# Kernel tuning notes

Measured on AMD Instinct MI355X. Metric: run time of the kernel, lower is better.

## Reference

```python
import jax, jax.numpy as jnp
import numpy as np

B, N, C = 32, 4097, 256  # N odd so threshold length (N+1)//2 == N//2+1 rfft bins
F = N // 2 + 1


def setup_inputs() -> dict:
    key = jax.random.key(0)
    k1, k2, k3, k4 = jax.random.split(key, 4)
    x_in = jax.random.normal(k1, (B, N, C), dtype=jnp.float32)
    # trunc_normal(std=0.02) ~ scaled normal for reference purposes
    complex_weight = jax.random.normal(k2, (C, 2), dtype=jnp.float32) * 0.02
    complex_weight_high = jax.random.normal(k3, (C, 2), dtype=jnp.float32) * 0.02
    threshold_param = jax.random.uniform(k4, (F,), dtype=jnp.float32)
    return {
        "x_in": x_in,
        "complex_weight": complex_weight,
        "complex_weight_high": complex_weight_high,
        "threshold_param": threshold_param,
    }


def reference(x_in, complex_weight, complex_weight_high, threshold_param):
    dtype = x_in.dtype
    x = x_in.astype(jnp.float32)
    x_fft = jnp.fft.rfft(x, axis=1, norm="ortho")  # [B, F, C] complex64

    weight = complex_weight[:, 0] + 1j * complex_weight[:, 1]  # [C]
    x_weighted = x_fft * weight

    # adaptive high-frequency mask (straight-through on threshold_param)
    energy = jnp.sum(jnp.abs(x_fft) ** 2, axis=-1)  # [B, F]
    median_energy = jnp.median(energy, axis=1, keepdims=True)  # [B, 1] (F odd -> exact middle, matches torch)
    normalized_energy = energy / (median_energy + 1e-6)
    hard = (normalized_energy > threshold_param).astype(jnp.float32)  # [B, F]
    adaptive_mask = jax.lax.stop_gradient(hard - threshold_param) + threshold_param

    weight_high = complex_weight_high[:, 0] + 1j * complex_weight_high[:, 1]  # [C]
    x_weighted = x_weighted + x_fft * adaptive_mask[..., None] * weight_high

    out = jnp.fft.irfft(x_weighted, n=N, axis=1, norm="ortho")  # [B, N, C]
    return out.astype(dtype)
```

## Files before the change

### kernel.cpp

```cpp
#include <hip/hip_runtime.h>
#include <math.h>
#include <float.h>

#define B_ 32
#define N_ 4097
#define C_ 256
#define F_ 2049
#define N2_ 241
#define Q_ 512
#define TWROWS 4352
#define INV_SQRT_N 0.0156230927f
#define W_N 0.0015336063f
#define W_17 0.36959913571644626f

typedef __attribute__((ext_vector_type(8))) short short8v;
typedef _Float16 f16x8 __attribute__((ext_vector_type(8)));
typedef __attribute__((ext_vector_type(4))) float f32x4;

#define C17T(r) ((r)==0 ? 1.0f : (r)==1 ? 0.9324722294f : (r)==2 ? 0.7390089172f : \
    (r)==3 ? 0.4457383558f : (r)==4 ? 0.0922683595f : (r)==5 ? -0.2736629901f : \
    (r)==6 ? -0.6026346364f : (r)==7 ? -0.8502171357f : (r)==8 ? -0.9829730997f : \
    (r)==9 ? -0.9829730997f : (r)==10 ? -0.8502171357f : (r)==11 ? -0.6026346364f : \
    (r)==12 ? -0.2736629901f : (r)==13 ? 0.0922683595f : (r)==14 ? 0.4457383558f : \
    (r)==15 ? 0.7390089172f : 0.9324722294f)
#define S17T(r) ((r)==0 ? 0.0f : (r)==1 ? 0.3612416662f : (r)==2 ? 0.6736956436f : \
    (r)==3 ? 0.8951632914f : (r)==4 ? 0.9957341763f : (r)==5 ? 0.9618256432f : \
    (r)==6 ? 0.7980172273f : (r)==7 ? 0.5264321629f : (r)==8 ? 0.1837495178f : \
    (r)==9 ? -0.1837495178f : (r)==10 ? -0.5264321629f : (r)==11 ? -0.7980172273f : \
    (r)==12 ? -0.9618256432f : (r)==13 ? -0.9957341763f : (r)==14 ? -0.8951632914f : \
    (r)==15 ? -0.6736956436f : -0.3612416662f)

__device__ __forceinline__ float bf2f(unsigned short u) {
    return __uint_as_float(((unsigned)u) << 16);
}
__device__ __forceinline__ unsigned short f2bf(float v) {
    unsigned u = __float_as_uint(v);
    u += 0x7FFFu + ((u >> 16) & 1u);
    return (unsigned short)(u >> 16);
}
__device__ __forceinline__ unsigned short f2h(float v) {
    union { _Float16 h; unsigned short u; } cv;
    cv.h = (_Float16)v;
    return cv.u;
}
__device__ __forceinline__ void gload16(const void* gptr, void* ldsptr) {
    __builtin_amdgcn_global_load_lds(
        (const __attribute__((address_space(1))) void*)gptr,
        (__attribute__((address_space(3))) void*)ldsptr,
        16, 0, 0);
}

__global__ __launch_bounds__(256, 4) void k_prep(const float* __restrict__ x,
                                                 unsigned short* __restrict__ yt,
                                                 unsigned short* __restrict__ twA,
                                                 unsigned short* __restrict__ twB) {
    int blk = blockIdx.x;
    int tid = threadIdx.x;
    if (blk >= 2048) {
        int base = (blk - 2048) * 4;
#pragma unroll
        for (int u = 0; u < 4; ++u) {
            int g = base + u;
            if (g < TWROWS) {
                int n = g, k2 = tid;
                unsigned pack = 0u;
                if (n <= 4096 && k2 <= 240) {
                    int rr = (n * k2) % N_;
                    float s, cth; sincosf(W_N * (float)rr, &s, &cth);
                    pack = (unsigned)f2bf(cth) | ((unsigned)f2bf(-s) << 16);
                }
                *(unsigned*)(twA + (size_t)n * Q_ + 2 * k2) = pack;
            } else {
                int i2 = g - TWROWS;
                int m = i2 & 255; int k1 = i2 >> 8;
                int n2 = tid;
                int t = m >> 1, r = m & 1;
                int f = k1 + 17 * t;
                unsigned ph = 0u;
                if (t <= 120 && f < F_ && n2 <= 240) {
                    float s_ = (k1 <= 8) ? 1.f : -1.f;
                    int rr = (f * n2) % N_;
                    float sn, cs; sincosf(W_N * (float)rr, &sn, &cs);
                    float a0 = (r == 0) ? cs : -sn;
                    float a1 = (r == 0) ? s_ * sn : s_ * cs;
                    ph = (unsigned)f2h(a0) | ((unsigned)f2h(a1) << 16);
                }
                size_t ub = ((size_t)(k1 * 256 + m)) * 256 + n2;
                *((unsigned*)twB + ub) = ph;
            }
        }
        return;
    }

    int b = blk >> 6; int rem = blk & 63;
    int n2t = rem >> 2, ct = rem & 3;
    int cl = tid & 63, sub = tid >> 6;
    int c = ct * 64 + cl;

    float ar[9][4], ai[8][4];
#pragma unroll
    for (int k = 0; k < 9; ++k)
#pragma unroll
        for (int i = 0; i < 4; ++i) ar[k][i] = 0.f;
#pragma unroll
    for (int k = 0; k < 8; ++k)
#pragma unroll
        for (int i = 0; i < 4; ++i) ai[k][i] = 0.f;

    const float* xb = x + (size_t)b * N_ * C_ + c;
#pragma unroll
    for (int n1 = 0; n1 < 17; ++n1) {
        float xv[4];
#pragma unroll
        for (int i = 0; i < 4; ++i) {
            int n2 = n2t * 16 + sub * 4 + i;
            xv[i] = (n2 <= 240) ? xb[(size_t)(n1 * N2_ + n2) * C_] : 0.f;
        }
#pragma unroll
        for (int k1 = 0; k1 < 9; ++k1) {
            const int r = (k1 * n1) % 17;
            const float cc = C17T(r), ss = S17T(r);
#pragma unroll
            for (int i = 0; i < 4; ++i) {
                ar[k1][i] += xv[i] * cc;
                if (k1 > 0) ai[k1 - 1][i] += xv[i] * ss;
            }
        }
    }

    __shared__ float lre[16 * 65], lim[16 * 65];
    int c2 = tid >> 2, qg = tid & 3;
#pragma unroll
    for (int j = 0; j < 9; ++j) {
        __syncthreads();
#pragma unroll
        for (int i = 0; i < 4; ++i) {
            int row = sub * 4 + i;
            lre[row * 65 + cl] = ar[j][i] * INV_SQRT_N;
            lim[row * 65 + cl] = (j > 0) ? (-ai[j - 1][i] * INV_SQRT_N) : 0.f;
        }
        __syncthreads();
        unsigned wh[4];
#pragma unroll
        for (int i = 0; i < 4; ++i) {
            int row = qg * 4 + i;
            float re = lre[row * 65 + c2], im = lim[row * 65 + c2];
            wh[i] = (unsigned)f2h(re) | ((unsigned)f2h(im) << 16);
        }
        size_t ubase = ((size_t)((b * 9 + j) * 256 + ct * 64 + c2)) * 256 + n2t * 16 + qg * 4;
        uint4 v0; v0.x = wh[0]; v0.y = wh[1]; v0.z = wh[2]; v0.w = wh[3];
        *(uint4*)((unsigned*)yt + ubase) = v0;
    }
}

__global__ __launch_bounds__(256) void k_stageB_v6(
        const unsigned short* __restrict__ yt, const unsigned short* __restrict__ twb,
        unsigned short* __restrict__ X, float* __restrict__ e2) {
    int bid = (blockIdx.x & 7) * 272 + (blockIdx.x >> 3);
    int b = bid / 68, rem = bid % 68;
    int j, mt, ct;
    if (rem < 4) { j = 0; mt = rem >> 1; ct = rem & 1; }
    else { int r2 = rem - 4; j = 1 + (r2 >> 3); int sub = r2 & 7; mt = sub >> 1; ct = sub & 1; }
    int k1 = (mt < 2) ? j : 17 - j;
    int mh = mt & 1;
    const unsigned short* pA = twb + (size_t)(k1 * 256 + mh * 128) * Q_;
    const unsigned short* pB = yt + (size_t)((b * 9 + j) * 256 + ct * 128) * Q_;

    int tid = threadIdx.x, lane = tid & 63, wid = tid >> 6;
    int wr = wid >> 1, wc = wid & 1;
    int l15 = lane & 15, lg = lane >> 4;
    int srow = lane >> 2, sch = lane & 3;

    __shared__ __align__(16) unsigned short lds[2][8192];
    __shared__ float eL[2][2][4][4][2];

    const unsigned short* gsrc[4];
#pragma unroll
    for (int r = 0; r < 4; ++r) {
        int row = (r & 1) * 64 + wid * 16 + srow;
        int ch = sch ^ ((row >> 1) & 3);
        gsrc[r] = ((r < 2) ? pA : pB) + (size_t)row * Q_ + ch * 8;
    }
    int aoff[4], boff[4];
#pragma unroll
    for (int rt = 0; rt < 4; ++rt) {
        int row = wr * 64 + rt * 16 + l15;
        aoff[rt] = row * 32 + (lg ^ ((row >> 1) & 3)) * 8;
    }
#pragma unroll
    for (int nt = 0; nt < 4; ++nt) {
        int row = wc * 64 + nt * 16 + l15;
        boff[nt] = 4096 + row * 32 + (lg ^ ((row >> 1) & 3)) * 8;
    }

    f32x4 acc[4][4];
#pragma unroll
    for (int rt = 0; rt < 4; ++rt)
#pragma unroll
        for (int nt = 0; nt < 4; ++nt) acc[rt][nt] = (f32x4){0.f, 0.f, 0.f, 0.f};

#define STAGE_B(bufi, q0) do {                                      \
        gload16(gsrc[0] + (q0), &lds[bufi][wid * 512]);             \
        gload16(gsrc[1] + (q0), &lds[bufi][2048 + wid * 512]);      \
        gload16(gsrc[2] + (q0), &lds[bufi][4096 + wid * 512]);      \
        gload16(gsrc[3] + (q0), &lds[bufi][6144 + wid * 512]);      \
    } while (0)

#define COMP_B(bufi) do {                                           \
        f16x8 a_[4], b_[4];                                         \
        _Pragma("unroll")                                           \
        for (int rt = 0; rt < 4; ++rt)                              \
            a_[rt] = *(const f16x8*)&lds[bufi][aoff[rt]];           \
        _Pragma("unroll")                                           \
        for (int nt = 0; nt < 4; ++nt)                              \
            b_[nt] = *(const f16x8*)&lds[bufi][boff[nt]];           \
        _Pragma("unroll")                                           \
        for (int rt = 0; rt < 4; ++rt)                              \
            _Pragma("unroll")                                       \
            for (int nt = 0; nt < 4; ++nt)                          \
                acc[rt][nt] = __builtin_amdgcn_mfma_f32_16x16x32_f16( \
                    a_[rt], b_[nt], acc[rt][nt], 0, 0, 0);          \
    } while (0)

    STAGE_B(0, 0);
    __syncthreads();
    for (int ks = 0; ks < 16; ks += 2) {
        STAGE_B(1, (ks + 1) * 32);
        COMP_B(0);
        __syncthreads();
        if (ks + 2 < 16) STAGE_B(0, (ks + 2) * 32);
        COMP_B(1);
        __syncthreads();
    }
#undef STAGE_B
#undef COMP_B

#pragma unroll
    for (int rt = 0; rt < 4; ++rt) {
        float e0 = 0.f, e1 = 0.f;
#pragma unroll
        for (int nt = 0; nt < 4; ++nt) {
            e0 += acc[rt][nt][0] * acc[rt][nt][0] + acc[rt][nt][1] * acc[rt][nt][1];
            e1 += acc[rt][nt][2] * acc[rt][nt][2] + acc[rt][nt][3] * acc[rt][nt][3];
        }
#pragma unroll
        for (int off = 1; off < 16; off <<= 1) {
            e0 += __shfl_xor(e0, off, 64);
            e1 += __shfl_xor(e1, off, 64);
        }
        if (l15 == 0) { eL[wr][wc][rt][lg][0] = e0; eL[wr][wc][rt][lg][1] = e1; }
    }
    __syncthreads();
    if (tid < 64) {
        int wr2 = tid >> 5, rt2 = (tid >> 3) & 3, lg2 = (tid >> 1) & 3, pr = tid & 1;
        int mrow = mh * 128 + wr2 * 64 + rt2 * 16 + lg2 * 4 + pr * 2;
        int f = k1 + 17 * (mrow >> 1);
        if (f < F_) {
            float e = eL[wr2][0][rt2][lg2][pr] + eL[wr2][1][rt2][lg2][pr];
            e2[(size_t)ct * (B_ * F_) + b * F_ + f] = e;
        }
    }

    unsigned short* st = (unsigned short*)lds;
#pragma unroll
    for (int rt = 0; rt < 4; ++rt) {
        __syncthreads();
#pragma unroll
        for (int nt = 0; nt < 4; ++nt)
#pragma unroll
            for (int jj = 0; jj < 4; ++jj) {
                int ri = wr * 16 + lg * 4 + jj;
                int col = wc * 64 + nt * 16 + l15;
                st[ri * 132 + col] = f2bf(acc[rt][nt][jj]);
            }
        __syncthreads();
#pragma unroll
        for (int rr = 0; rr < 8; ++rr) {
            int ri = wid * 8 + rr;
            int mrow = mh * 128 + (ri >> 4) * 64 + rt * 16 + (ri & 15);
            int t = mrow >> 1, p = mrow & 1;
            int f = k1 + 17 * t;
            if (f < F_) {
                unsigned v = *(unsigned*)&st[ri * 132 + 2 * lane];
                *(unsigned*)(X + ((size_t)((b * F_ + f) * 2 + p)) * C_ + ct * 128 + 2 * lane) = v;
            }
        }
    }
}

__global__ __launch_bounds__(256) void k_median(const float* __restrict__ e2,
                                                float* __restrict__ med) {
    int b = blockIdx.x, tid = threadIdx.x;
    __shared__ unsigned vals[F_];
    __shared__ unsigned hist[256];
    __shared__ unsigned scanbuf[256];
    __shared__ unsigned sh_prefix;
    __shared__ int sh_rank;
    for (int i = tid; i < F_; i += 256)
        vals[i] = __float_as_uint(e2[b * F_ + i] + e2[(size_t)B_ * F_ + b * F_ + i]);
    if (tid == 0) { sh_prefix = 0u; sh_rank = 1024; }
    __syncthreads();
#pragma unroll
    for (int shift = 24; shift >= 0; shift -= 8) {
        hist[tid] = 0u;
        __syncthreads();
        unsigned prefix = sh_prefix;
        unsigned hmask = (shift == 24) ? 0u : (0xFFFFFFFFu << (shift + 8));
        for (int i = tid; i < F_; i += 256) {
            unsigned v = vals[i];
            if (((v ^ prefix) & hmask) == 0u)
                atomicAdd(&hist[(v >> shift) & 255], 1u);
        }
        __syncthreads();
        scanbuf[tid] = hist[tid];
        __syncthreads();
#pragma unroll
        for (int off = 1; off < 256; off <<= 1) {
            unsigned y = (tid >= off) ? scanbuf[tid - off] : 0u;
            __syncthreads();
            scanbuf[tid] += y;
            __syncthreads();
        }
        int rank = sh_rank;
        unsigned cumP = (tid == 0) ? 0u : scanbuf[tid - 1];
        unsigned cumI = scanbuf[tid];
        __syncthreads();
        if ((unsigned)rank >= cumP && (unsigned)rank < cumI) {
            sh_prefix = prefix | ((unsigned)tid << shift);
            sh_rank = rank - (int)cumP;
        }
        __syncthreads();
    }
    if (tid == 0) med[b] = __uint_as_float(sh_prefix);
}

__global__ __launch_bounds__(256) void k_vbuild_t(
        const unsigned short* __restrict__ X, const float* __restrict__ e2,
        const float* __restrict__ med, const float* __restrict__ thr,
        const float* __restrict__ cw, const float* __restrict__ cwh,
        unsigned short* __restrict__ vt) {
    int bid = blockIdx.x;
    int b = bid >> 7; int rem = bid & 127;
    int kt = rem >> 3, ct = rem & 7;
    int tid = threadIdx.x;
    int cl = tid & 31, ks = tid >> 5;
    int c = ct * 32 + cl;

    __shared__ unsigned stage[17 * 32 * 17];

    float wr = cw[2 * c], wi = cw[2 * c + 1];
    float whr = cwh[2 * c], whi = cwh[2 * c + 1];
    float denom = med[b] + 1e-6f;

#pragma unroll
    for (int kk = 0; kk < 2; ++kk) {
        int klocal = kk * 8 + ks;
        int k2 = kt * 16 + klocal;
        float vr[17], vi[17];
#pragma unroll
        for (int m = 0; m < 17; ++m) { vr[m] = 0.f; vi[m] = 0.f; }
        if (k2 <= 240) {
#pragma unroll
            for (int s = 0; s < 9; ++s) {
                int f = k2 + 241 * s;
                if (f < F_) {
                    float e = e2[b * F_ + f] + e2[(size_t)B_ * F_ + b * F_ + f];
                    float m = (e / denom > thr[f]) ? 1.0f : 0.0f;
                    float wer = wr + m * whr, wei = wi + m * whi;
                    float cf = ((f == 0) ? 1.0f : 2.0f) * INV_SQRT_N;
                    const unsigned short* Xrow = X + ((size_t)(b * F_ + f) * 2) * C_;
                    float Xr = bf2f(Xrow[c]), Xi = bf2f(Xrow[C_ + c]);
                    float Zr = (Xr * wer - Xi * wei) * cf;
                    float Zi = (Xr * wei + Xi * wer) * cf;
#pragma unroll
                    for (int m2 = 0; m2 < 17; ++m2) {
                        const int r = (s * m2) % 17;
                        vr[m2] += Zr * C17T(r) - Zi * S17T(r);
                        vi[m2] += Zr * S17T(r) + Zi * C17T(r);
                    }
                }
            }
        }
#pragma unroll
        for (int m2 = 0; m2 < 17; ++m2)
            stage[(m2 * 32 + cl) * 17 + klocal] =
                (unsigned)f2bf(vr[m2]) | ((unsigned)f2bf(vi[m2]) << 16);
    }
    __syncthreads();
    unsigned* vt32 = (unsigned*)vt;
    for (int r = tid; r < 544; r += 256) {
        int m2 = r >> 5, c2 = r & 31;
        size_t ubase = ((size_t)((b * 17 + m2) * 256 + ct * 32 + c2)) * 256 + kt * 16;
        const unsigned* srow = &stage[(m2 * 32 + c2) * 17];
#pragma unroll
        for (int g = 0; g < 4; ++g) {
            uint4 w;
            w.x = srow[g * 4]; w.y = srow[g * 4 + 1];
            w.z = srow[g * 4 + 2]; w.w = srow[g * 4 + 3];
            *(uint4*)(vt32 + ubase + g * 4) = w;
        }
    }
}

__global__ __launch_bounds__(256) void k_stageC_v4(const short* __restrict__ vt,
                                                   const short* __restrict__ twA,
                                                   float* __restrict__ out) {
    int bid = (blockIdx.x & 7) * 272 + (blockIdx.x >> 3);
    int b = bid / 68, rem = bid % 68;
    int m2 = rem >> 2, mt = (rem >> 1) & 1, ct = rem & 1;

    int tid = threadIdx.x, lane = tid & 63, wid = tid >> 6;
    int wr = wid >> 1, wc = wid & 1;
    int l15 = lane & 15, lg = lane >> 4;
    int srow = lane >> 2, sch = lane & 3;

    const short* vtb = vt + (size_t)((b * 17 + m2) * 256 + ct * 128) * Q_;

    __shared__ __align__(16) short lds[2][8192];

    const short* gsrc[4];
#pragma unroll
    for (int r = 0; r < 4; ++r) {
        int row = (r & 1) * 64 + wid * 16 + srow;
        int ch = sch ^ ((row >> 1) & 3);
        if (r < 2) {
            int n = 17 * (mt * 128 + row) + m2;
            gsrc[r] = twA + (size_t)n * Q_ + ch * 8;
        } else {
            gsrc[r] = vtb + (size_t)row * Q_ + ch * 8;
        }
    }
    int aoff[4], boff[4];
#pragma unroll
    for (int rt = 0; rt < 4; ++rt) {
        int row = wr * 64 + rt * 16 + l15;
        aoff[rt] = row * 32 + (lg ^ ((row >> 1) & 3)) * 8;
    }
#pragma unroll
    for (int nt = 0; nt < 4; ++nt) {
        int row = wc * 64 + nt * 16 + l15;
        boff[nt] = 4096 + row * 32 + (lg ^ ((row >> 1) & 3)) * 8;
    }

    f32x4 acc[4][4];
#pragma unroll
    for (int rt = 0; rt < 4; ++rt)
#pragma unroll
        for (int nt = 0; nt < 4; ++nt) acc[rt][nt] = (f32x4){0.f, 0.f, 0.f, 0.f};

#define STAGE_C(bufi, q0) do {                                      \
        gload16(gsrc[0] + (q0), &lds[bufi][wid * 512]);             \
        gload16(gsrc[1] + (q0), &lds[bufi][2048 + wid * 512]);      \
        gload16(gsrc[2] + (q0), &lds[bufi][4096 + wid * 512]);      \
        gload16(gsrc[3] + (q0), &lds[bufi][6144 + wid * 512]);      \
    } while (0)

#define COMP_C(bufi) do {                                           \
        short8v a_[4], b_[4];                                       \
        _Pragma("unroll")                                           \
        for (int rt = 0; rt < 4; ++rt)                              \
            a_[rt] = *(const short8v*)&lds[bufi][aoff[rt]];         \
        _Pragma("unroll")                                           \
        for (int nt = 0; nt < 4; ++nt)                              \
            b_[nt] = *(const short8v*)&lds[bufi][boff[nt]];         \
        _Pragma("unroll")                                           \
        for (int rt = 0; rt < 4; ++rt)                              \
            _Pragma("unroll")                                       \
            for (int nt = 0; nt < 4; ++nt)                          \
                acc[rt][nt] = __builtin_amdgcn_mfma_f32_16x16x32_bf16( \
                    a_[rt], b_[nt], acc[rt][nt], 0, 0, 0);          \
    } while (0)

    STAGE_C(0, 0);
    __syncthreads();
    for (int ks = 0; ks < 16; ks += 2) {
        STAGE_C(1, (ks + 1) * 32);
        COMP_C(0);
        __syncthreads();
        if (ks + 2 < 16) STAGE_C(0, (ks + 2) * 32);
        COMP_C(1);
        __syncthreads();
    }
#undef STAGE_C
#undef COMP_C

    float* fl = (float*)lds;
#pragma unroll
    for (int rt = 0; rt < 4; ++rt) {
        __syncthreads();
#pragma unroll
        for (int nt = 0; nt < 4; ++nt)
#pragma unroll
            for (int jj = 0; jj < 4; ++jj) {
                int ri = wr * 16 + lg * 4 + jj;
                int col = wc * 64 + nt * 16 + l15;
                fl[ri * 130 + col] = acc[rt][nt][jj];
            }
        __syncthreads();
#pragma unroll
        for (int rr = 0; rr < 8; ++rr) {
            int ri = wid * 8 + rr;
            int m1 = mt * 128 + (ri >> 4) * 64 + rt * 16 + (ri & 15);
            if (m1 < N2_) {
                int n = 17 * m1 + m2;
                float2 v = *(float2*)&fl[ri * 130 + 2 * lane];
                *(float2*)(out + ((size_t)b * N_ + n) * C_ + ct * 128 + 2 * lane) = v;
            }
        }
    }
}

extern "C" void kernel_launch(void* const* d_in, const int* in_sizes, int n_in,
                              void* d_out, int out_size, void* d_ws, size_t ws_size,
                              hipStream_t stream) {
    const float* x   = (const float*)d_in[0];
    const float* cw  = (const float*)d_in[1];
    const float* cwh = (const float*)d_in[2];
    const float* thr = (const float*)d_in[3];
    float* out = (float*)d_out;

    char* ws = (char*)d_ws;
    unsigned short* Xb    = (unsigned short*)ws;
    char* sh = ws + 67141632ull;
    unsigned short* yt    = (unsigned short*)sh;
    unsigned short* vtb   = (unsigned short*)sh;
    char* tail = sh + 142606336ull;
    unsigned short* twA   = (unsigned short*)tail;
    unsigned short* twB   = (unsigned short*)(tail + 4456448ull);
    float* e2  = (float*)(tail + 8912896ull);
    float* med = (float*)(tail + 8912896ull + 524544ull);

    k_prep<<<4224, 256, 0, stream>>>(x, yt, twA, twB);
    k_stageB_v6<<<B_ * 68, 256, 0, stream>>>(yt, twB, Xb, e2);
    k_median<<<B_, 256, 0, stream>>>(e2, med);
    k_vbuild_t<<<B_ * 128, 256, 0, stream>>>(Xb, e2, med, thr, cw, cwh, vtb);
    k_stageC_v4<<<B_ * 68, 256, 0, stream>>>((const short*)vtb, (const short*)twA, out);
}
```

Before: 295.1 us.

## Widen stage C tile to all 256 channels and batch prep LDS transposes

Stage C now computes a 128x256 output tile per block instead of 128x128, so each twiddle A tile is loaded once for both channel halves. This halves the grid and makes the output stores 16-byte wide. The cost is a larger accumulator (32 MFMA tiles per wave) and 48KB of LDS, with launch_bounds(256,2) set to keep occupancy. Separately, the prep kernel's transpose now stages three frequency rows per sync round instead of one, cutting barriers from 18 to 6 at the price of more shared memory.

```diff
diff --git a/kernel.cpp b/kernel.cpp
--- a/kernel.cpp
+++ b/kernel.cpp
@@ -128,28 +128,37 @@
         }
     }
 
-    __shared__ float lre[16 * 65], lim[16 * 65];
+    __shared__ float lre[3 * 16 * 68], lim[3 * 16 * 68];
     int c2 = tid >> 2, qg = tid & 3;
 #pragma unroll
-    for (int j = 0; j < 9; ++j) {
-        __syncthreads();
-#pragma unroll
-        for (int i = 0; i < 4; ++i) {
-            int row = sub * 4 + i;
-            lre[row * 65 + cl] = ar[j][i] * INV_SQRT_N;
-            lim[row * 65 + cl] = (j > 0) ? (-ai[j - 1][i] * INV_SQRT_N) : 0.f;
-        }
-        __syncthreads();
-        unsigned wh[4];
-#pragma unroll
-        for (int i = 0; i < 4; ++i) {
-            int row = qg * 4 + i;
-            float re = lre[row * 65 + c2], im = lim[row * 65 + c2];
-            wh[i] = (unsigned)f2h(re) | ((unsigned)f2h(im) << 16);
-        }
-        size_t ubase = ((size_t)((b * 9 + j) * 256 + ct * 64 + c2)) * 256 + n2t * 16 + qg * 4;
-        uint4 v0; v0.x = wh[0]; v0.y = wh[1]; v0.z = wh[2]; v0.w = wh[3];
-        *(uint4*)((unsigned*)yt + ubase) = v0;
+    for (int g = 0; g < 3; ++g) {
+        __syncthreads();
+#pragma unroll
+        for (int jj = 0; jj < 3; ++jj) {
+            int j = g * 3 + jj;
+#pragma unroll
+            for (int i = 0; i < 4; ++i) {
+                int row = sub * 4 + i;
+                lre[(jj * 16 + row) * 68 + cl] = ar[j][i] * INV_SQRT_N;
+                lim[(jj * 16 + row) * 68 + cl] = (j > 0) ? (-ai[j - 1][i] * INV_SQRT_N) : 0.f;
+            }
+        }
+        __syncthreads();
+#pragma unroll
+        for (int jj = 0; jj < 3; ++jj) {
+            int j = g * 3 + jj;
+            unsigned wh[4];
+#pragma unroll
+            for (int i = 0; i < 4; ++i) {
+                int row = qg * 4 + i;
+                float re = lre[(jj * 16 + row) * 68 + c2];
+                float im = lim[(jj * 16 + row) * 68 + c2];
+                wh[i] = (unsigned)f2h(re) | ((unsigned)f2h(im) << 16);
+            }
+            size_t ubase = ((size_t)((b * 9 + j) * 256 + ct * 64 + c2)) * 256 + n2t * 16 + qg * 4;
+            uint4 v0; v0.x = wh[0]; v0.y = wh[1]; v0.z = wh[2]; v0.w = wh[3];
+            *(uint4*)((unsigned*)yt + ubase) = v0;
+        }
     }
 }
 
@@ -402,71 +411,75 @@
     }
 }
 
-__global__ __launch_bounds__(256) void k_stageC_v4(const short* __restrict__ vt,
-                                                   const short* __restrict__ twA,
-                                                   float* __restrict__ out) {
-    int bid = (blockIdx.x & 7) * 272 + (blockIdx.x >> 3);
-    int b = bid / 68, rem = bid % 68;
-    int m2 = rem >> 2, mt = (rem >> 1) & 1, ct = rem & 1;
+__global__ __launch_bounds__(256, 2) void k_stageC_v5(const short* __restrict__ vt,
+                                                      const short* __restrict__ twA,
+                                                      float* __restrict__ out) {
+    int bid = (blockIdx.x & 7) * 136 + (blockIdx.x >> 3);
+    int b = bid / 34, rem = bid % 34;
+    int m2 = rem >> 1, mt = rem & 1;
 
     int tid = threadIdx.x, lane = tid & 63, wid = tid >> 6;
     int wr = wid >> 1, wc = wid & 1;
     int l15 = lane & 15, lg = lane >> 4;
     int srow = lane >> 2, sch = lane & 3;
 
-    const short* vtb = vt + (size_t)((b * 17 + m2) * 256 + ct * 128) * Q_;
-
-    __shared__ __align__(16) short lds[2][8192];
-
-    const short* gsrc[4];
-#pragma unroll
-    for (int r = 0; r < 4; ++r) {
-        int row = (r & 1) * 64 + wid * 16 + srow;
-        int ch = sch ^ ((row >> 1) & 3);
+    const short* vtb = vt + (size_t)((b * 17 + m2) * 256) * Q_;
+
+    __shared__ __align__(16) short lds[2][12288];
+
+    const short* gsrc[6];
+#pragma unroll
+    for (int r = 0; r < 6; ++r) {
         if (r < 2) {
+            int row = r * 64 + wid * 16 + srow;
+            int ch = sch ^ ((row >> 1) & 3);
             int n = 17 * (mt * 128 + row) + m2;
             gsrc[r] = twA + (size_t)n * Q_ + ch * 8;
         } else {
+            int row = (r - 2) * 64 + wid * 16 + srow;
+            int ch = sch ^ ((row >> 1) & 3);
             gsrc[r] = vtb + (size_t)row * Q_ + ch * 8;
         }
     }
-    int aoff[4], boff[4];
+    int aoff[4], boff[8];
 #pragma unroll
     for (int rt = 0; rt < 4; ++rt) {
         int row = wr * 64 + rt * 16 + l15;
         aoff[rt] = row * 32 + (lg ^ ((row >> 1) & 3)) * 8;
     }
 #pragma unroll
-    for (int nt = 0; nt < 4; ++nt) {
-        int row = wc * 64 + nt * 16 + l15;
+    for (int nt = 0; nt < 8; ++nt) {
+        int row = wc * 128 + nt * 16 + l15;
         boff[nt] = 4096 + row * 32 + (lg ^ ((row >> 1) & 3)) * 8;
     }
 
-    f32x4 acc[4][4];
+    f32x4 acc[4][8];
 #pragma unroll
     for (int rt = 0; rt < 4; ++rt)
 #pragma unroll
-        for (int nt = 0; nt < 4; ++nt) acc[rt][nt] = (f32x4){0.f, 0.f, 0.f, 0.f};
+        for (int nt = 0; nt < 8; ++nt) acc[rt][nt] = (f32x4){0.f, 0.f, 0.f, 0.f};
 
 #define STAGE_C(bufi, q0) do {                                      \
         gload16(gsrc[0] + (q0), &lds[bufi][wid * 512]);             \
         gload16(gsrc[1] + (q0), &lds[bufi][2048 + wid * 512]);      \
         gload16(gsrc[2] + (q0), &lds[bufi][4096 + wid * 512]);      \
         gload16(gsrc[3] + (q0), &lds[bufi][6144 + wid * 512]);      \
+        gload16(gsrc[4] + (q0), &lds[bufi][8192 + wid * 512]);      \
+        gload16(gsrc[5] + (q0), &lds[bufi][10240 + wid * 512]);     \
     } while (0)
 
 #define COMP_C(bufi) do {                                           \
-        short8v a_[4], b_[4];                                       \
+        short8v a_[4], b_[8];                                       \
         _Pragma("unroll")                                           \
         for (int rt = 0; rt < 4; ++rt)                              \
             a_[rt] = *(const short8v*)&lds[bufi][aoff[rt]];         \
         _Pragma("unroll")                                           \
-        for (int nt = 0; nt < 4; ++nt)                              \
+        for (int nt = 0; nt < 8; ++nt)                              \
             b_[nt] = *(const short8v*)&lds[bufi][boff[nt]];         \
         _Pragma("unroll")                                           \
         for (int rt = 0; rt < 4; ++rt)                              \
             _Pragma("unroll")                                       \
-            for (int nt = 0; nt < 4; ++nt)                          \
+            for (int nt = 0; nt < 8; ++nt)                          \
                 acc[rt][nt] = __builtin_amdgcn_mfma_f32_16x16x32_bf16( \
                     a_[rt], b_[nt], acc[rt][nt], 0, 0, 0);          \
     } while (0)
@@ -489,12 +502,12 @@
     for (int rt = 0; rt < 4; ++rt) {
         __syncthreads();
 #pragma unroll
-        for (int nt = 0; nt < 4; ++nt)
+        for (int nt = 0; nt < 8; ++nt)
 #pragma unroll
             for (int jj = 0; jj < 4; ++jj) {
                 int ri = wr * 16 + lg * 4 + jj;
-                int col = wc * 64 + nt * 16 + l15;
-                fl[ri * 130 + col] = acc[rt][nt][jj];
+                int col = wc * 128 + nt * 16 + l15;
+                fl[ri * 260 + col] = acc[rt][nt][jj];
             }
         __syncthreads();
 #pragma unroll
@@ -503,8 +516,8 @@
             int m1 = mt * 128 + (ri >> 4) * 64 + rt * 16 + (ri & 15);
             if (m1 < N2_) {
                 int n = 17 * m1 + m2;
-                float2 v = *(float2*)&fl[ri * 130 + 2 * lane];
-                *(float2*)(out + ((size_t)b * N_ + n) * C_ + ct * 128 + 2 * lane) = v;
+                float4 v = *(float4*)&fl[ri * 260 + 4 * lane];
+                *(float4*)(out + ((size_t)b * N_ + n) * C_ + 4 * lane) = v;
             }
         }
     }
@@ -534,5 +547,5 @@
     k_stageB_v6<<<B_ * 68, 256, 0, stream>>>(yt, twB, Xb, e2);
     k_median<<<B_, 256, 0, stream>>>(e2, med);
     k_vbuild_t<<<B_ * 128, 256, 0, stream>>>(Xb, e2, med, thr, cw, cwh, vtb);
-    k_stageC_v4<<<B_ * 68, 256, 0, stream>>>((const short*)vtb, (const short*)twA, out);
-}
+    k_stageC_v5<<<B_ * 34, 256, 0, stream>>>((const short*)vtb, (const short*)twA, out);
+}
```

New measurement: 291.1 us. About the same (-1.3%).
